# Kernel optimization log

Measured on AMD Instinct MI355X. Metric: run time of the kernel, lower is better.

The kernel has to match this reference:

```python
import jax, jax.numpy as jnp
import numpy as np

TOTAL_BITS = 16
FRAC_BITS = 8
SCALE = 2.0 ** FRAC_BITS
QMIN = -(2.0 ** (TOTAL_BITS - 1)) / SCALE
QMAX = (2.0 ** (TOTAL_BITS - 1) - 1) / SCALE


def quant(x):
    # fixed-point quantize: round to frac_bits, clamp to total_bits range (STE grad)
    q = jnp.clip(jnp.round(x * SCALE) / SCALE, QMIN, QMAX)
    return x + jax.lax.stop_gradient(q - x)


def hard_sigmoid(x):
    return jnp.clip(x / 6.0 + 0.5, 0.0, 1.0)


def hard_tanh(x):
    return jnp.clip(x, -1.0, 1.0)


def setup_inputs() -> dict:
    key = jax.random.key(0)
    ks = jax.random.split(key, 7)
    B, T, I, H, O = 256, 512, 128, 256, 1
    return {
        "x": jax.random.normal(ks[0], (B, T, I), jnp.float32),
        "w_ih": jax.random.normal(ks[1], (4 * H, I), jnp.float32) * 0.05,
        "w_hh": jax.random.normal(ks[2], (4 * H, H), jnp.float32) * 0.05,
        "b_ih": jax.random.normal(ks[3], (4 * H,), jnp.float32) * 0.05,
        "b_hh": jax.random.normal(ks[4], (4 * H,), jnp.float32) * 0.05,
        "w_lin": jax.random.normal(ks[5], (O, H), jnp.float32) * 0.05,
        "b_lin": jax.random.normal(ks[6], (O,), jnp.float32) * 0.05,
    }


def reference(x, w_ih, w_hh, b_ih, b_hh, w_lin, b_lin):
    B, T, I = x.shape
    H = w_hh.shape[1]
    xq = quant(x)
    w_ih_q, w_hh_q = quant(w_ih), quant(w_hh)
    b_ih_q, b_hh_q = quant(b_ih), quant(b_hh)
    # input projection for all timesteps at once: [B,T,4H]
    gi = quant(jnp.einsum("bti,gi->btg", xq, w_ih_q) + b_ih_q)

    def step(carry, gi_t):
        h, c = carry
        gh = quant(h @ w_hh_q.T + b_hh_q)
        g = quant(gi_t + gh)
        i_g, f_g, c_g, o_g = jnp.split(g, 4, axis=-1)
        i_g = quant(hard_sigmoid(i_g))
        f_g = quant(hard_sigmoid(f_g))
        c_g = quant(hard_tanh(c_g))
        o_g = quant(hard_sigmoid(o_g))
        c_new = quant(quant(f_g * c) + quant(i_g * c_g))
        h_new = quant(o_g * quant(hard_tanh(c_new)))
        return (h_new, c_new), None

    h0 = jnp.zeros((B, H), x.dtype)
    c0 = jnp.zeros((B, H), x.dtype)
    (h_last, _), _ = jax.lax.scan(step, (h0, c0), jnp.swapaxes(gi, 0, 1))
    # x[:, -1] of the LSTM output == h_last; fixed-point linear head
    return quant(h_last @ quant(w_lin).T + quant(b_lin))
```

## Files before the change

### kernel.cpp

```cpp
#include <hip/hip_runtime.h>
#include <stdint.h>
#include <stddef.h>

typedef int i32x4 __attribute__((ext_vector_type(4)));
typedef int i32x2 __attribute__((ext_vector_type(2)));

#define WS_WFRAG   0u
#define WS_WIH     262144u
#define WS_BIASHH  393216u
#define WS_BIASIH  397312u
#define WS_WLIN    401408u
#define WS_BLIN    402432u
#define WS_HSTATE  409600u
#define WS_CSTATE  540672u
#define WS_GI      1064960u

#define MFMA_I8(a,b,c) __builtin_amdgcn_mfma_i32_16x16x64_i8(a,b,c,0,0,0)
#define RHE8(x) ((((x) + 127) + (((x) >> 8) & 1)) >> 8)

#define DPPX1(v)   __builtin_amdgcn_update_dpp(0, (v), 0xB1, 0xF, 0xF, true)
#define DPPX2(v)   __builtin_amdgcn_update_dpp(0, (v), 0x4E, 0xF, 0xF, true)
#define DPPROR8(v) __builtin_amdgcn_update_dpp(0, (v), 0x128, 0xF, 0xF, true)

#define BAR() do { asm volatile("s_waitcnt lgkmcnt(0)" ::: "memory"); \
                   __builtin_amdgcn_s_barrier(); } while (0)

__device__ __forceinline__ float clamp3(float x, float lo, float hi) {
    return __builtin_amdgcn_fmed3f(x, lo, hi);
}
__device__ __forceinline__ float q16f(float x) {
    return clamp3(__builtin_rintf(x * 256.0f), -32768.0f, 32767.0f);
}
__device__ __forceinline__ int iclamp(int v, int lo, int hi) {
    return v < lo ? lo : (v > hi ? hi : v);
}
__device__ __forceinline__ int sigq(int u) {
    int q = __mul24(u, 43691) >> 18;
    int r = u - __mul24(q, 6);
    return q + (((r + (q & 1)) > 3) ? 1 : 0);
}

__global__ void prep_kernel(const float* __restrict__ wih, const float* __restrict__ whh,
                            const float* __restrict__ bih, const float* __restrict__ bhh,
                            const float* __restrict__ wlin, const float* __restrict__ blin,
                            uint8_t* __restrict__ ws) {
    int tid = blockIdx.x * blockDim.x + threadIdx.x;
    {
        int p = tid;
        int j = p & 15, lane = (p >> 4) & 63, ks = (p >> 10) & 3, t8 = (p >> 12) & 7, w = (p >> 15) & 7;
        int row = (t8 >> 1) * 256 + w * 32 + (t8 & 1) * 16 + (lane & 15);
        int k = ks * 64 + (lane >> 4) * 16 + j;
        int v = (int)q16f(whh[row * 256 + k]);
        v = iclamp(v, -127, 127);
        ((int8_t*)(ws + WS_WFRAG))[p] = (int8_t)v;
    }
    if (tid < 131072) {
        int gcol = tid >> 7, k = tid & 127;
        int v = (int)q16f(wih[gcol * 128 + k]);
        v = iclamp(v, -127, 127);
        ((int8_t*)(ws + WS_WIH))[tid] = (int8_t)v;
    }
    if (tid < 1024) {
        ((int*)(ws + WS_BIASHH))[tid] = ((int)q16f(bhh[tid])) * 256;
        ((int*)(ws + WS_BIASIH))[tid] = ((int)q16f(bih[tid])) * 256;
    }
    if (tid < 256) ((int*)(ws + WS_WLIN))[tid] = (int)q16f(wlin[tid]);
    if (tid == 0)  ((int*)(ws + WS_BLIN))[0]   = (int)q16f(blin[0]);
}

__launch_bounds__(512, 2)
__global__ void gi_kernel(const float* __restrict__ x, uint8_t* __restrict__ ws, int t0) {
    __shared__ uint8_t xa[2][2048], xb[2][2048];
    int tid = threadIdx.x;
    int wgr = blockIdx.x;
    int tlb = blockIdx.y * 4;
    int wid = tid >> 6, lane = tid & 63, lr = lane & 15, lg = lane >> 4;

    const uint8_t* wq = ws + WS_WIH;
    i32x4 af[8][2];
#pragma unroll
    for (int mt = 0; mt < 8; ++mt) {
        int gcol = (mt >> 1) * 256 + wid * 32 + (mt & 1) * 16 + lr;
#pragma unroll
        for (int kt = 0; kt < 2; ++kt)
            af[mt][kt] = *(const i32x4*)(wq + gcol * 128 + kt * 64 + lg * 16);
    }
    i32x4 bcv[8];
    const int* bi = (const int*)(ws + WS_BIASIH);
#pragma unroll
    for (int mt = 0; mt < 8; ++mt) {
        int gb = (mt >> 1) * 256 + wid * 32 + (mt & 1) * 16 + lg * 4;
        bcv[mt] = *(const i32x4*)(bi + gb);
    }

    auto STAGE = [&](int tl, int buf) {
        int row = tid >> 5, c4 = (tid & 31) * 4;
        int b = wgr * 16 + row;
        const float4 xv = *(const float4*)(x + ((size_t)b * 512 + (t0 + tl)) * 128 + c4);
        int v0 = (int)q16f(xv.x), v1 = (int)q16f(xv.y), v2 = (int)q16f(xv.z), v3 = (int)q16f(xv.w);
        uint32_t da = ((uint32_t)((v0 >> 7) & 255)) | ((uint32_t)((v1 >> 7) & 255) << 8) |
                      ((uint32_t)((v2 >> 7) & 255) << 16) | ((uint32_t)((v3 >> 7) & 255) << 24);
        uint32_t db = ((uint32_t)(v0 & 127)) | ((uint32_t)(v1 & 127) << 8) |
                      ((uint32_t)(v2 & 127) << 16) | ((uint32_t)(v3 & 127) << 24);
        int addr = row * 128 + (((c4 >> 4) ^ (row & 7)) * 16) + (c4 & 15);
        *(uint32_t*)(&xa[buf][0] + addr) = da;
        *(uint32_t*)(&xb[buf][0] + addr) = db;
    };

    STAGE(tlb, 0);
    __syncthreads();

    for (int s4 = 0; s4 < 4; ++s4) {
        int tl = tlb + s4;
        if (s4 < 3) STAGE(tl + 1, (s4 + 1) & 1);
        int buf = s4 & 1;

        i32x4 bha[2], bhb[2];
#pragma unroll
        for (int kt = 0; kt < 2; ++kt) {
            int addr = lr * 128 + ((((kt * 4) + lg) ^ (lr & 7)) * 16);
            bha[kt] = *(const i32x4*)(&xa[buf][0] + addr);
            bhb[kt] = *(const i32x4*)(&xb[buf][0] + addr);
        }
        i32x4 acch[8], accl[8];
#pragma unroll
        for (int mt = 0; mt < 8; ++mt) {
            i32x4 z = {0, 0, 0, 0};
            acch[mt] = MFMA_I8(af[mt][0], bha[0], z);
            accl[mt] = MFMA_I8(af[mt][0], bhb[0], bcv[mt]);
            acch[mt] = MFMA_I8(af[mt][1], bha[1], acch[mt]);
            accl[mt] = MFMA_I8(af[mt][1], bhb[1], accl[mt]);
        }
        int gq[8][4];
#pragma unroll
        for (int mt = 0; mt < 8; ++mt)
#pragma unroll
            for (int rr = 0; rr < 4; ++rr) {
                int v = acch[mt][rr] * 128 + accl[mt][rr];
                gq[mt][rr] = iclamp(RHE8(v), -32768, 32767);
            }
        unsigned batch = (unsigned)(wgr * 16 + lr);
#pragma unroll
        for (int mm2 = 0; mm2 < 2; ++mm2)
#pragma unroll
            for (int rr2 = 0; rr2 < 4; ++rr2) {
                i32x2 outv;
                outv[0] = (gq[mm2][rr2] & 0xFFFF)     | (gq[4 + mm2][rr2] << 16);
                outv[1] = (gq[2 + mm2][rr2] & 0xFFFF) | (gq[6 + mm2][rr2] << 16);
                int Lp = ((rr2 & 1) << 1) | (mm2 << 2) | ((rr2 >> 1) << 3) | (lg << 4);
                *(i32x2*)(ws + WS_GI + (size_t)tl * 524288u +
                          (size_t)((batch * 8u + (unsigned)wid) * 64u + (unsigned)Lp) * 4u) = outv;
            }
        __syncthreads();
    }
}

__launch_bounds__(512, 2)
__global__ void recur_kernel(uint8_t* __restrict__ ws, float* __restrict__ out, int t0, int cs) {
    __shared__ __align__(16) uint8_t hbuf[2][512];
    __shared__ long long redl[8];
    int tid = threadIdx.x, w = tid >> 6, lane = tid & 63;
    int wb = blockIdx.x;
    int gsel = lane & 1;
    int cp   = (lane >> 1) & 1;
    int mm   = (lane >> 2) & 1;
    int X    = (lane >> 3) & 1;
    int sg   = lane >> 4;
    uint8_t* hb0 = &hbuf[0][0];

    i32x4 wf[8][4];
#pragma unroll
    for (int t8 = 0; t8 < 8; ++t8)
#pragma unroll
        for (int ks = 0; ks < 4; ++ks)
            wf[t8][ks] = *(const i32x4*)(ws + WS_WFRAG + (((unsigned)(w * 8 + t8) * 4 + ks) << 10) + lane * 16);

    int addrB[4];
#pragma unroll
    for (int ks = 0; ks < 4; ++ks)
        addrB[ks] = ks * 128 + cp * 64 + sg * 16;

    int k_own = w * 32 + mm * 16 + sg * 4 + 2 * X + cp;
    int addrW4 = (w >> 1) * 128 + gsel * 64 + ((w & 1) * 2 + mm) * 16 + sg * 4;
    int hsh = 8 * (2 * X + cp);
    int biasP[2], wlv;
    {
        const int* bhh256 = (const int*)(ws + WS_BIASHH);
        int G0 = gsel, G1 = gsel + 2;
        biasP[0] = bhh256[G0 * 256 + k_own] + 768 * 256;
        biasP[1] = bhh256[G1 * 256 + k_own] + (G1 == 2 ? 0 : 768 * 256);
        wlv = ((const int*)(ws + WS_WLIN))[k_own];
    }
    size_t gioff = (size_t)((unsigned)wb * 8u + (unsigned)w) * 256u + (unsigned)lane * 4u;

    uint8_t* hst = ws + WS_HSTATE + (unsigned)wb * 512u;
    int* cst = (int*)(ws + WS_CSTATE) + (unsigned)wb * 512u + (unsigned)tid;

    int c_;
    if (t0 == 0) {
        c_ = 0;
        if (tid < 128) *(uint32_t*)(hb0 + tid * 4) = 0u;
    } else {
        c_ = *cst;
        if (tid < 128) *(uint32_t*)(hb0 + tid * 4) = *(const uint32_t*)(hst + tid * 4);
    }
    int gcur = *(const int*)(ws + WS_GI + gioff);
    int gnx;
    __syncthreads();

    int hl_ = 0;
    const i32x4 zerov = {0, 0, 0, 0};

#define PLANEPAIR(T0, T1, T2, T3, U, V)                                                \
    int U, V;                                                                          \
    {                                                                                  \
        int ua = X ? acc[T0][2] : acc[T0][0], va = X ? acc[T0][3] : acc[T0][1];        \
        int ub = X ? acc[T1][2] : acc[T1][0], vb = X ? acc[T1][3] : acc[T1][1];        \
        int uc = X ? acc[T2][2] : acc[T2][0], vc = X ? acc[T2][3] : acc[T2][1];        \
        int ud = X ? acc[T3][2] : acc[T3][0], vd = X ? acc[T3][3] : acc[T3][1];        \
        int u0 = mm ? ub : ua, v0 = mm ? vb : va;                                      \
        int u1 = mm ? ud : uc, v1 = mm ? vd : vc;                                      \
        U = gsel ? u1 : u0;                                                            \
        V = gsel ? v1 : v0;                                                            \
    }
#define SLOT(U, V, BIAS, OUTG)                                                         \
    int OUTG;                                                                          \
    {                                                                                  \
        int own = cp ? V : U;                                                          \
        int snd = cp ? U : V;                                                          \
        int z = DPPX2(snd);                                                            \
        int hi = cp ? z : own;                                                         \
        int lo = cp ? own : z;                                                         \
        OUTG = RHE8(hi * 4 + lo + (BIAS));                                             \
    }
#define STEP(PP, GUSE, GPRE, TPRE)                                                     \
    {                                                                                  \
        GPRE = *(const int*)(ws + WS_GI + (size_t)(TPRE) * 524288u + gioff);           \
        i32x4 bfv[4];                                                                  \
        _Pragma("unroll")                                                              \
        for (int ks = 0; ks < 4; ++ks)                                                 \
            bfv[ks] = *(const i32x4*)(hb0 + (PP) * 512 + addrB[ks]);                   \
        __builtin_amdgcn_s_setprio(1);                                                 \
        i32x4 acc[8];                                                                  \
        _Pragma("unroll")                                                              \
        for (int ks = 0; ks < 4; ++ks) {                                               \
            _Pragma("unroll")                                                          \
            for (int t8 = 0; t8 < 4; ++t8)                                             \
                acc[t8] = (ks == 0) ? MFMA_I8(wf[t8][0], bfv[0], zerov)                \
                                    : MFMA_I8(wf[t8][ks], bfv[ks], acc[t8]);           \
        }                                                                              \
        PLANEPAIR(0, 1, 2, 3, uA, vA)                                                  \
        SLOT(uA, vA, biasP[0], gA)                                                     \
        int givlo = ((GUSE) << 16) >> 16, givhi = (GUSE) >> 16;                        \
        int first = sigq(iclamp(gA + givlo, 0, 1536));         \
        int p_f = RHE8(__mul24(first, c_));                            \
        _Pragma("unroll")                                                              \
        for (int ks = 0; ks < 4; ++ks) {                                               \
            _Pragma("unroll")                                                          \
            for (int t8 = 4; t8 < 8; ++t8)                                             \
                acc[t8] = (ks == 0) ? MFMA_I8(wf[t8][0], bfv[0], zerov)                \
                                    : MFMA_I8(wf[t8][ks], bfv[ks], acc[t8]);           \
        }                                                                              \
        __builtin_amdgcn_s_setprio(0);                                                 \
        PLANEPAIR(4, 5, 6, 7, uB, vB)                                                  \
        SLOT(uB, vB, biasP[1], gB)                                                     \
        int gBs = gB + givhi;                                                          \
        int sigB = sigq(iclamp(gBs, 0, 1536));                                         \
        int clpB = iclamp(gBs, -256, 256);                                             \
        int second = gsel ? sigB : clpB;                       \
        int p_i = RHE8(__mul24(first, second));                        \
        int ownp = gsel ? p_f : p_i;                                                   \
        int othp = DPPX1(ownp);                                                        \
        int cn  = iclamp(ownp + othp, -32768, 32767);                                  \
        c_ = cn;                                                                       \
        int th = iclamp(cn, -256, 256);                                                \
        int hq1 = RHE8(__mul24(second, th));                      \
        int hqp = DPPX1(hq1);                                                          \
        int hq = gsel ? hq1 : hqp;                                                     \
               \
        unsigned hby = (unsigned)(gsel ? (hq & 3) : (hq >> 2)) & 255u;                 \
        unsigned pv = hby << hsh;                                                      \
        pv |= (unsigned)DPPX2((int)pv);                                                \
        pv |= (unsigned)DPPROR8((int)pv);                                              \
        if ((lane & 10) == 0)                                                          \
            *(uint32_t*)(hb0 + ((PP) ^ 1) * 512 + addrW4) = pv;                        \
        hl_ = hq;                                                                      \
        BAR();                                                                         \
    }

    for (int tl = 0; tl < cs; tl += 2) {
        int tn2 = (tl + 2 < cs) ? tl + 2 : 0;
        STEP(0, gcur, gnx, tl + 1)
        STEP(1, gnx, gcur, tn2)
    }
#undef STEP
#undef SLOT
#undef PLANEPAIR

    if (tid < 128) *(uint32_t*)(hst + tid * 4) = *(const uint32_t*)(hb0 + tid * 4);
    *cst = c_;

    if (t0 + cs == 512) {
        long long s = gsel ? 0LL : (long long)hl_ * (long long)wlv;
        s += __shfl_xor(s, 1);
        s += __shfl_xor(s, 2);
        s += __shfl_xor(s, 4);
        s += __shfl_xor(s, 8);
        s += __shfl_xor(s, 16);
        s += __shfl_xor(s, 32);
        if (lane == 0) redl[w] = s;
        __syncthreads();
        if (tid == 0) {
            long long tot = 0;
#pragma unroll
            for (int ww = 0; ww < 8; ++ww) tot += redl[ww];
            tot += 256LL * (long long)((const int*)(ws + WS_BLIN))[0];
            long long q = ((tot + 127) + ((tot >> 8) & 1)) >> 8;
            q = q < -32768 ? -32768 : (q > 32767 ? 32767 : q);
            out[wb] = (float)q * 0.00390625f;
        }
    }
}

extern "C" void kernel_launch(void* const* d_in, const int* in_sizes, int n_in,
                              void* d_out, int out_size, void* d_ws, size_t ws_size,
                              hipStream_t stream) {
    const float* x    = (const float*)d_in[0];
    const float* wih  = (const float*)d_in[1];
    const float* whh  = (const float*)d_in[2];
    const float* bih  = (const float*)d_in[3];
    const float* bhh  = (const float*)d_in[4];
    const float* wlin = (const float*)d_in[5];
    const float* blin = (const float*)d_in[6];
    float* out = (float*)d_out;
    uint8_t* ws = (uint8_t*)d_ws;

    prep_kernel<<<512, 512, 0, stream>>>(wih, whh, bih, bhh, wlin, blin, ws);

    int cs = 512;
    while ((size_t)WS_GI + (size_t)cs * 524288u > ws_size && cs > 8) cs >>= 1;

    for (int t0 = 0; t0 < 512; t0 += cs) {
        gi_kernel<<<dim3(16, cs / 4), 512, 0, stream>>>(x, ws, t0);
        recur_kernel<<<256, 512, 0, stream>>>(ws, out, t0, cs);
    }
}
```

Measured before the change: 516.8 us.

## Replace per-step block barrier with per-wave LDS progress flags and k-slice polling

Removes the workgroup-wide barrier at the end of each recurrent step. Each wave instead publishes its step counter in a shared progress array. Consumers spin-wait only on the pair of waves that produced the k-slice of the hidden state they are about to load. The MFMA loop is reordered to iterate over k-slices in the outer loop, so matrix work on early slices can start while later slices are still being produced. This trades barrier stalls for LDS spin polling and relies on volatile accesses and waitcnt for ordering, which makes the memory-ordering correctness more delicate.

New measurement: 663.6 us. +28.4%, slower.

```diff
diff --git a/kernel.cpp b/kernel.cpp
--- a/kernel.cpp
+++ b/kernel.cpp
@@ -21,9 +21,6 @@
 #define DPPX1(v)   __builtin_amdgcn_update_dpp(0, (v), 0xB1, 0xF, 0xF, true)
 #define DPPX2(v)   __builtin_amdgcn_update_dpp(0, (v), 0x4E, 0xF, 0xF, true)
 #define DPPROR8(v) __builtin_amdgcn_update_dpp(0, (v), 0x128, 0xF, 0xF, true)
-
-#define BAR() do { asm volatile("s_waitcnt lgkmcnt(0)" ::: "memory"); \
-                   __builtin_amdgcn_s_barrier(); } while (0)
 
 __device__ __forceinline__ float clamp3(float x, float lo, float hi) {
     return __builtin_amdgcn_fmed3f(x, lo, hi);
@@ -158,6 +155,7 @@
 __launch_bounds__(512, 2)
 __global__ void recur_kernel(uint8_t* __restrict__ ws, float* __restrict__ out, int t0, int cs) {
     __shared__ __align__(16) uint8_t hbuf[2][512];
+    __shared__ __align__(16) uint16_t prog16[16];
     __shared__ long long redl[8];
     int tid = threadIdx.x, w = tid >> 6, lane = tid & 63;
     int wb = blockIdx.x;
@@ -204,12 +202,23 @@
         c_ = *cst;
         if (tid < 128) *(uint32_t*)(hb0 + tid * 4) = *(const uint32_t*)(hst + tid * 4);
     }
+    if (tid < 16) prog16[tid] = 0;
     int gcur = *(const int*)(ws + WS_GI + gioff);
     int gnx;
     __syncthreads();
 
     int hl_ = 0;
     const i32x4 zerov = {0, 0, 0, 0};
+
+#define POLLPAIR(KS, TL)                                                               \
+    {                                                                                  \
+        uint32_t need_ = (uint32_t)(TL);                                               \
+        while (true) {                                                                 \
+            uint32_t pp_ = *(volatile const uint32_t*)&prog16[2 * (KS)];               \
+            if ((pp_ & 0xffffu) >= need_ && (pp_ >> 16) >= need_) break;               \
+        }                                                                              \
+        asm volatile("" ::: "memory");                                                 \
+    }
 
 #define PLANEPAIR(T0, T1, T2, T3, U, V)                                                \
     int U, V;                                                                          \
@@ -233,34 +242,35 @@
         int lo = cp ? own : z;                                                         \
         OUTG = RHE8(hi * 4 + lo + (BIAS));                                             \
     }
-#define STEP(PP, GUSE, GPRE, TPRE)                                                     \
+#define STEP(PP, GUSE, GPRE, TPRE, TL)                                                 \
     {                                                                                  \
         GPRE = *(const int*)(ws + WS_GI + (size_t)(TPRE) * 524288u + gioff);           \
+        i32x4 acc[8];                                                                  \
         i32x4 bfv[4];                                                                  \
-        _Pragma("unroll")                                                              \
-        for (int ks = 0; ks < 4; ++ks)                                                 \
-            bfv[ks] = *(const i32x4*)(hb0 + (PP) * 512 + addrB[ks]);                   \
+        POLLPAIR(0, TL)                                                                \
+        bfv[0] = *(const i32x4*)(hb0 + (PP) * 512 + addrB[0]);                         \
+        POLLPAIR(1, TL)                                                                \
+        bfv[1] = *(const i32x4*)(hb0 + (PP) * 512 + addrB[1]);                         \
         __builtin_amdgcn_s_setprio(1);                                                 \
-        i32x4 acc[8];                                                                  \
-        _Pragma("unroll")                                                              \
-        for (int ks = 0; ks < 4; ++ks) {                                               \
-            _Pragma("unroll")                                                          \
-            for (int t8 = 0; t8 < 4; ++t8)                                             \
-                acc[t8] = (ks == 0) ? MFMA_I8(wf[t8][0], bfv[0], zerov)                \
-                                    : MFMA_I8(wf[t8][ks], bfv[ks], acc[t8]);           \
-        }                                                                              \
+        _Pragma("unroll")                                                              \
+        for (int t8 = 0; t8 < 8; ++t8) acc[t8] = MFMA_I8(wf[t8][0], bfv[0], zerov);    \
+        POLLPAIR(2, TL)                                                                \
+        bfv[2] = *(const i32x4*)(hb0 + (PP) * 512 + addrB[2]);                         \
+        _Pragma("unroll")                                                              \
+        for (int t8 = 0; t8 < 8; ++t8) acc[t8] = MFMA_I8(wf[t8][1], bfv[1], acc[t8]);  \
+        POLLPAIR(3, TL)                                                                \
+        bfv[3] = *(const i32x4*)(hb0 + (PP) * 512 + addrB[3]);                         \
+        _Pragma("unroll")                                                              \
+        for (int t8 = 0; t8 < 8; ++t8) acc[t8] = MFMA_I8(wf[t8][2], bfv[2], acc[t8]);  \
+        _Pragma("unroll")                                                              \
+        for (int t8 = 0; t8 < 4; ++t8) acc[t8] = MFMA_I8(wf[t8][3], bfv[3], acc[t8]);  \
         PLANEPAIR(0, 1, 2, 3, uA, vA)                                                  \
         SLOT(uA, vA, biasP[0], gA)                                                     \
         int givlo = ((GUSE) << 16) >> 16, givhi = (GUSE) >> 16;                        \
         int first = sigq(iclamp(gA + givlo, 0, 1536));         \
         int p_f = RHE8(__mul24(first, c_));                            \
         _Pragma("unroll")                                                              \
-        for (int ks = 0; ks < 4; ++ks) {                                               \
-            _Pragma("unroll")                                                          \
-            for (int t8 = 4; t8 < 8; ++t8)                                             \
-                acc[t8] = (ks == 0) ? MFMA_I8(wf[t8][0], bfv[0], zerov)                \
-                                    : MFMA_I8(wf[t8][ks], bfv[ks], acc[t8]);           \
-        }                                                                              \
+        for (int t8 = 4; t8 < 8; ++t8) acc[t8] = MFMA_I8(wf[t8][3], bfv[3], acc[t8]);  \
         __builtin_amdgcn_s_setprio(0);                                                 \
         PLANEPAIR(4, 5, 6, 7, uB, vB)                                                  \
         SLOT(uB, vB, biasP[1], gB)                                                     \
@@ -285,17 +295,22 @@
         if ((lane & 10) == 0)                                                          \
             *(uint32_t*)(hb0 + ((PP) ^ 1) * 512 + addrW4) = pv;                        \
         hl_ = hq;                                                                      \
-        BAR();                                                                         \
+        asm volatile("s_waitcnt lgkmcnt(0)" ::: "memory");                             \
+        if (lane == 0) *(volatile uint16_t*)&prog16[w] = (uint16_t)((TL) + 1);         \
+        asm volatile("" ::: "memory");                                                 \
     }
 
     for (int tl = 0; tl < cs; tl += 2) {
         int tn2 = (tl + 2 < cs) ? tl + 2 : 0;
-        STEP(0, gcur, gnx, tl + 1)
-        STEP(1, gnx, gcur, tn2)
+        STEP(0, gcur, gnx, tl + 1, tl)
+        STEP(1, gnx, gcur, tn2, tl + 1)
     }
 #undef STEP
 #undef SLOT
 #undef PLANEPAIR
+#undef POLLPAIR
+
+    __syncthreads();
 
     if (tid < 128) *(uint32_t*)(hst + tid * 4) = *(const uint32_t*)(hb0 + tid * 4);
     *cst = c_;
```
